# Kernel optimization log

Hardware: AMD Instinct MI355X
Metric: run time of the kernel (lower is better)

The kernel has to match this reference:

```python
import jax, jax.numpy as jnp
import numpy as np

N = 8192       # num_nodes
DEG = 16       # edges per node
E = N * DEG    # num_edges
F = 128        # num_features
R = 20         # num_rbf_features
L = 3          # num_message_passing_layers
CUT = 3.0      # cutoff_dist


def setup_inputs() -> dict:
    key = jax.random.key(0)
    ks = jax.random.split(key, 18)
    atoms = jax.random.randint(ks[0], (N,), 1, 119)
    # every node appears as a destination exactly DEG times -> bincount > 0
    idx_i = jnp.repeat(jnp.arange(N), DEG)
    idx_j = jax.random.randint(ks[1], (E,), 0, N)
    raw = jax.random.normal(ks[2], (E, 3), jnp.float32)
    rel_dir = raw / jnp.linalg.norm(raw, axis=-1, keepdims=True)
    rel_dist = jax.random.uniform(ks[3], (E,), jnp.float32, 0.1, CUT - 1e-3)
    emb = (jax.random.normal(ks[4], (119, F), jnp.float32) / np.sqrt(F)).at[0].set(0.0)
    def w(k, shape, fan_in):
        return jax.random.normal(k, shape, jnp.float32) / np.sqrt(fan_in)
    return {
        'atoms': atoms, 'idx_i': idx_i, 'idx_j': idx_j,
        'rel_dir': rel_dir, 'rel_dist': rel_dist, 'emb': emb,
        'msg_w1': w(ks[5], (L, F, F), F), 'msg_b1': jnp.zeros((L, F), jnp.float32),
        'msg_w2': w(ks[6], (L, F, 3 * F), F), 'msg_b2': jnp.zeros((L, 3 * F), jnp.float32),
        'rbf_w': w(ks[7], (L, R, 3 * F), R), 'rbf_b': jnp.zeros((L, 3 * F), jnp.float32),
        'Uw': w(ks[8], (L, F, F), F), 'Vw': w(ks[9], (L, F, F), F),
        'upd_w1': w(ks[10], (L, 2 * F, F), 2 * F), 'upd_b1': jnp.zeros((L, F), jnp.float32),
        'upd_w2': w(ks[11], (L, F, 3 * F), F), 'upd_b2': jnp.zeros((L, 3 * F), jnp.float32),
    }


def painn_forward(atoms, idx_i, idx_j, rel_dir, rel_dist, emb,
                  msg_w1, msg_b1, msg_w2, msg_b2, rbf_w, rbf_b,
                  Uw, Vw, upd_w1, upd_b1, upd_w2, upd_b2):
    silu = jax.nn.silu
    # cosine cutoff and sinusoidal RBF features of edge distances
    cut = 0.5 * (jnp.cos(jnp.pi * rel_dist / CUT) + 1.0)               # [E]
    n = jnp.arange(1, R + 1, dtype=rel_dist.dtype)
    rbf = jnp.sin(n * jnp.pi * rel_dist[:, None] / CUT) / rel_dist[:, None]  # [E,R]

    s = emb[atoms]                                   # [N,F]
    v = jnp.zeros((N, F, 3), s.dtype)                # [N,F,3]
    counts = jax.ops.segment_sum(jnp.ones(E, s.dtype), idx_i, num_segments=N)  # bincount

    for l in range(L):
        # ---- message block ----
        phi = silu(s @ msg_w1[l] + msg_b1[l]) @ msg_w2[l] + msg_b2[l]  # [N,3F]
        W = (rbf @ rbf_w[l] + rbf_b[l]) * cut[:, None]                 # [E,3F]
        phi_W = phi[idx_j] * W                                         # [E,3F]
        p_vv, p_ss, p_vs = jnp.split(phi_W, 3, axis=-1)
        ds = jax.ops.segment_sum(p_ss, idx_i, num_segments=N) / counts[:, None]
        ve = v[idx_j] * p_vv[..., None] + p_vs[..., None] * rel_dir[:, None, :]  # [E,F,3]
        dv = jax.ops.segment_sum(ve, idx_i, num_segments=N) / counts[:, None, None]
        s = s + ds
        v = v + dv
        # ---- update block ----
        Uv = jnp.einsum('nfc,fg->ngc', v, Uw[l])       # [N,F,3]
        Vv = jnp.einsum('nfc,fg->ngc', v, Vw[l])       # [N,F,3]
        a_in = jnp.concatenate([jnp.linalg.norm(Vv, axis=-1), s], axis=-1)  # [N,2F]
        a = silu(a_in @ upd_w1[l] + upd_b1[l]) @ upd_w2[l] + upd_b2[l]      # [N,3F]
        a_vv, a_sv, a_ss = jnp.split(a, 3, axis=-1)
        s = s + a_ss + a_sv * jnp.sum(Uv * Vv, axis=-1)
        v = v + Uv * a_vv[..., None]
    return s, v


def reference(atoms, idx_i, idx_j, rel_dir, rel_dist, emb,
              msg_w1, msg_b1, msg_w2, msg_b2, rbf_w, rbf_b,
              Uw, Vw, upd_w1, upd_b1, upd_w2, upd_b2):
    return painn_forward(atoms, idx_i, idx_j, rel_dir, rel_dist, emb,
                         msg_w1, msg_b1, msg_w2, msg_b2, rbf_w, rbf_b,
                         Uw, Vw, upd_w1, upd_b1, upd_w2, upd_b2)
```

## Files before the change

kernel.cpp:

```cpp
#include <hip/hip_runtime.h>
#include <hip/hip_fp16.h>

#define N_NODES 8192
#define DEG     16
#define NEDGE   (N_NODES*DEG)
#define F       128
#define F3      384
#define RBF     20
#define NLAYER  3
#define NF      (N_NODES*F)
#define PI_F    3.14159265358979f

typedef unsigned short u16;
typedef __bf16 bf16x8 __attribute__((ext_vector_type(8)));
typedef float  f32x4  __attribute__((ext_vector_type(4)));
typedef _Float16 f16x2 __attribute__((ext_vector_type(2)));

__device__ __forceinline__ float bf2f(u16 u){ return __uint_as_float(((unsigned)u)<<16); }
__device__ __forceinline__ u16 f2bf(float f){
  unsigned x = __float_as_uint(f);
  unsigned r = (x + 0x7FFFu + ((x>>16)&1u)) >> 16;
  return (u16)r;
}
__device__ __forceinline__ float lo_bf(unsigned u){ return __uint_as_float(u<<16); }
__device__ __forceinline__ float hi_bf(unsigned u){ return __uint_as_float(u & 0xFFFF0000u); }
__device__ __forceinline__ float silu_f(float x){ return x / (1.f + __expf(-x)); }
__device__ __forceinline__ float ldsrc(const void* src, int i, int bf){
  return bf ? bf2f(((const u16*)src)[i]) : ((const float*)src)[i];
}
__device__ __forceinline__ unsigned packh2(float a, float b){
  return (unsigned)__half_as_ushort(__float2half(a)) |
         ((unsigned)__half_as_ushort(__float2half(b)) << 16);
}
__device__ __forceinline__ float fdot2u(unsigned a, unsigned b, float c){
  return __builtin_amdgcn_fdot2(__builtin_bit_cast(f16x2, a),
                                __builtin_bit_cast(f16x2, b), c, false);
}

__global__ void k_detect(const u16* __restrict__ rd, int* __restrict__ flag){
  if (threadIdx.x == 0 && blockIdx.x == 0){
    int ok = 1;
    for (int i = 0; i < 128; i++){
      float v = bf2f(rd[2*i]);
      if (!(v > 0.01f && v < 4.0f)) { ok = 0; break; }
    }
    *flag = ok;
  }
}

__device__ __forceinline__ void splitw(const void* src, u16* bh, u16* bl,
                                       int i, int K, int Ncol, int bf){
  int kn = K*Ncol; int l = i/kn; int r = i - l*kn; int k = r/Ncol; int n = r - k*Ncol;
  float w = ldsrc(src, i, bf);
  u16 h = f2bf(w);
  size_t o = (size_t)l*kn + (size_t)n*K + k;
  bh[o] = h; bl[o] = f2bf(w - bf2f(h));
}

__global__ __launch_bounds__(256) void k_prep(
    const void* mb1, const void* mb2, const void* b1, const void* b2,
    const void* rw,  const void* rb,
    const void* mw1, const void* mw2, const void* w1, const void* w2,
    const void* Uw,  const void* Vw,
    const void* dist, const void* dirv, const int* __restrict__ idxj,
    const int* __restrict__ atoms, const void* __restrict__ emb,
    float* c_mb1, float* c_mb2, float* c_b1, float* c_b2,
    unsigned* rwp2,
    u16* mw1h, u16* mw1l, u16* mw2h, u16* mw2l, u16* w1h, u16* w1l,
    u16* w2h, u16* w2l, u16* uvh, u16* uvl,
    uint4* edata,
    float* s, u16* s_h, u16* s_l,
    u16* p0h, u16* p0l, u16* bufA16, u16* bufB16,
    const int* __restrict__ flag){
  int i = blockIdx.x*256 + threadIdx.x;
  int bf = *flag;
  const int S0=NLAYER*F, S1=NLAYER*F3, S2=NLAYER*F, S3=NLAYER*F3;
  const int S4=NLAYER*11*F3;
  const int S5=NLAYER*F*F, S6=NLAYER*F*F3, S7=NLAYER*2*F*F, S8=NLAYER*F*F3, S9=NLAYER*256*F;
  if (i < S0){ c_mb1[i]=ldsrc(mb1,i,bf); return; } i-=S0;
  if (i < S1){ c_mb2[i]=ldsrc(mb2,i,bf); return; } i-=S1;
  if (i < S2){ c_b1[i] =ldsrc(b1, i,bf); return; } i-=S2;
  if (i < S3){ c_b2[i] =ldsrc(b2, i,bf); return; } i-=S3;
  if (i < S4){
    int l = i/(11*F3); int r = i - l*(11*F3); int r2 = r/F3; int col = r - r2*F3;
    float w0, w1v;
    if (r2 < 10){
      w0  = ldsrc(rw, (l*RBF + 2*r2  )*F3 + col, bf);
      w1v = ldsrc(rw, (l*RBF + 2*r2+1)*F3 + col, bf);
    } else {
      w0  = ldsrc(rb, l*F3 + col, bf);
      w1v = 0.f;
    }
    rwp2[i] = packh2(w0, w1v);
    return;
  } i-=S4;
  if (i < S5){ splitw(mw1, mw1h, mw1l, i, F,   F,  bf); return; } i-=S5;
  if (i < S6){ splitw(mw2, mw2h, mw2l, i, F,   F3, bf); return; } i-=S6;
  if (i < S7){ splitw(w1,  w1h,  w1l,  i, 2*F, F,  bf); return; } i-=S7;
  if (i < S8){ splitw(w2,  w2h,  w2l,  i, F,   F3, bf); return; } i-=S8;
  if (i < S9){
    int l=i/(256*F); int r=i-l*(256*F); int n=r>>7; int k=r&127;
    int si=(l*F+k)*F+(n&127);
    float w = ldsrc((n<128)?Uw:Vw, si, bf);
    u16 h=f2bf(w); uvh[i]=h; uvl[i]=f2bf(w-bf2f(h));
    return;
  } i-=S9;
  if (i < NEDGE){
    int e = i;
    float d = ldsrc(dist, e, bf);
    float cut = 0.5f*(cosf(PI_F*d*(1.f/3.f)) + 1.0f);
    float ic = cut/d;
    unsigned o[16];
    #pragma unroll
    for (int r2=0;r2<10;r2++){
      float s0 = sinf((2*r2+1)*PI_F*d*(1.f/3.f))*ic;
      float s1 = sinf((2*r2+2)*PI_F*d*(1.f/3.f))*ic;
      o[r2] = packh2(s0, s1);
    }
    o[10] = packh2(cut, 0.f);
    o[11] = __float_as_uint(ldsrc(dirv, e*3+0, bf));
    o[12] = __float_as_uint(ldsrc(dirv, e*3+1, bf));
    o[13] = __float_as_uint(ldsrc(dirv, e*3+2, bf));
    o[14] = (unsigned)idxj[e];
    o[15] = 0;
    uint4* dst = edata + (size_t)e*4;
    dst[0] = make_uint4(o[0],o[1],o[2],o[3]);
    dst[1] = make_uint4(o[4],o[5],o[6],o[7]);
    dst[2] = make_uint4(o[8],o[9],o[10],o[11]);
    dst[3] = make_uint4(o[12],o[13],o[14],o[15]);
    return;
  } i-=NEDGE;
  if (i < NF){
    int n = i >> 7, f = i & 127;
    float sv = ldsrc(emb, atoms[n]*F + f, bf);
    s[i] = sv;
    u16 hb = f2bf(sv); s_h[i] = hb; s_l[i] = f2bf(sv - bf2f(hb));
    p0h[i]=0; p0h[NF+i]=0; p0h[2*(size_t)NF+i]=0;
    p0l[i]=0; p0l[NF+i]=0; p0l[2*(size_t)NF+i]=0;
    bufA16[(size_t)i*4+2]=0; bufA16[(size_t)i*4+3]=0;
    bufB16[(size_t)i*2+1]=0;
  }
}
#define PREP_TOTAL (NLAYER*(F+F3+F+F3+11*F3+F*F+F*F3+2*F*F+F*F3+256*F) + NEDGE + NF)

__global__ __launch_bounds__(256) void k_msg(const u16* __restrict__ s_h,
                                             const u16* __restrict__ s_l,
                                             const u16* __restrict__ w1h_,
                                             const u16* __restrict__ w1l_,
                                             const u16* __restrict__ w2h_,
                                             const u16* __restrict__ w2l_,
                                             const float* __restrict__ b1,
                                             const float* __restrict__ b2,
                                             u16* __restrict__ bufA16,
                                             u16* __restrict__ bufB16){
  __shared__ u16 Ah[16*136], Al[16*136];
  __shared__ u16 Hh[16*136], Hl[16*136];
  __shared__ u16 Bh[64*136], Bl[64*136];
  int t = threadIdx.x, lane = t&63, w = t>>6;
  int row0 = blockIdx.x<<4;
  int l15 = lane&15, q8 = (lane>>4)<<3, qrow = (lane>>4)<<2;

  #pragma unroll
  for (int q=0;q<2;q++){
    int id = t + 256*q; int pl = id>>8, rem = id&255, r = rem>>4, c = (rem&15)<<3;
    *(uint4*)((pl?Al:Ah)+r*136+c) = *(const uint4*)((pl?s_l:s_h) + (size_t)(row0+r)*F + c);
  }

  for (int cg=0;cg<2;cg++){
    __syncthreads();
    #pragma unroll
    for (int q=0;q<8;q++){
      int id = t + 256*q; int pl = id>>10, rem = id&1023, r = rem>>4, c = (rem&15)<<3;
      *(uint4*)((pl?Bl:Bh)+r*136+c) = *(const uint4*)((pl?w1l_:w1h_) + (size_t)(cg*64+r)*F + c);
    }
    __syncthreads();
    f32x4 acc; acc[0]=0;acc[1]=0;acc[2]=0;acc[3]=0;
    #pragma unroll
    for (int k0=0;k0<F;k0+=32){
      bf16x8 a_h = *(const bf16x8*)&Ah[l15*136 + k0 + q8];
      bf16x8 a_l = *(const bf16x8*)&Al[l15*136 + k0 + q8];
      bf16x8 b_h = *(const bf16x8*)&Bh[(w*16+l15)*136 + k0 + q8];
      bf16x8 b_l = *(const bf16x8*)&Bl[(w*16+l15)*136 + k0 + q8];
      acc = __builtin_amdgcn_mfma_f32_16x16x32_bf16(a_h, b_h, acc, 0,0,0);
      acc = __builtin_amdgcn_mfma_f32_16x16x32_bf16(a_h, b_l, acc, 0,0,0);
      acc = __builtin_amdgcn_mfma_f32_16x16x32_bf16(a_l, b_h, acc, 0,0,0);
    }
    int col = cg*64 + w*16 + l15;
    float bb = b1[col];
    #pragma unroll
    for (int r=0;r<4;r++){
      float val = silu_f(acc[r] + bb);
      u16 hb = f2bf(val);
      Hh[(qrow+r)*136 + col] = hb;
      Hl[(qrow+r)*136 + col] = f2bf(val - bf2f(hb));
    }
  }

  for (int cg=0;cg<6;cg++){
    __syncthreads();
    #pragma unroll
    for (int q=0;q<8;q++){
      int id = t + 256*q; int pl = id>>10, rem = id&1023, r = rem>>4, c = (rem&15)<<3;
      *(uint4*)((pl?Bl:Bh)+r*136+c) = *(const uint4*)((pl?w2l_:w2h_) + (size_t)(cg*64+r)*F + c);
    }
    __syncthreads();
    f32x4 acc; acc[0]=0;acc[1]=0;acc[2]=0;acc[3]=0;
    #pragma unroll
    for (int k0=0;k0<F;k0+=32){
      bf16x8 a_h = *(const bf16x8*)&Hh[l15*136 + k0 + q8];
      bf16x8 a_l = *(const bf16x8*)&Hl[l15*136 + k0 + q8];
      bf16x8 b_h = *(const bf16x8*)&Bh[(w*16+l15)*136 + k0 + q8];
      bf16x8 b_l = *(const bf16x8*)&Bl[(w*16+l15)*136 + k0 + q8];
      acc = __builtin_amdgcn_mfma_f32_16x16x32_bf16(a_h, b_h, acc, 0,0,0);
      acc = __builtin_amdgcn_mfma_f32_16x16x32_bf16(a_h, b_l, acc, 0,0,0);
      acc = __builtin_amdgcn_mfma_f32_16x16x32_bf16(a_l, b_h, acc, 0,0,0);
    }
    int gc = cg*64 + w*16 + l15;
    float bb = b2[gc];
    #pragma unroll
    for (int r=0;r<4;r++){
      int grow = row0 + qrow + r;
      u16 v = f2bf(acc[r] + bb);
      size_t rowo = (size_t)grow*F;
      if (gc < F)        bufA16[(rowo + gc)*4 + 0]     = v;
      else if (gc < 2*F) bufA16[(rowo + gc - F)*4 + 1] = v;
      else               bufB16[(rowo + gc - 2*F)*2]   = v;
    }
  }
}

__global__ __launch_bounds__(256) void k_agg(const uint4* __restrict__ ed_g,
                                             const uint2* __restrict__ bufA,
                                             const unsigned* __restrict__ bufB,
                                             const unsigned* __restrict__ rwp2,
                                             const u16* __restrict__ vi_h,
                                             const u16* __restrict__ vi_l,
                                             u16* __restrict__ vo_h,
                                             u16* __restrict__ vo_l,
                                             float* __restrict__ s,
                                             u16* __restrict__ s_h,
                                             u16* __restrict__ s_l){
  __shared__ uint4 ed4[128];
  int t = threadIdx.x;
  int half = t >> 7, f = t & 127;

  unsigned rw2[3][11];
  #pragma unroll
  for (int r2=0;r2<11;r2++){
    rw2[0][r2] = rwp2[r2*F3 + f];
    rw2[1][r2] = rwp2[r2*F3 + F + f];
    rw2[2][r2] = rwp2[r2*F3 + 2*F + f];
  }

  int nA = blockIdx.x * 2;
  if (t < 128) ed4[t] = ed_g[(size_t)nA*64 + t];
  __syncthreads();

  int n = nA + half;
  int base = half*64;
  float ds=0.f, dv0=0.f, dv1=0.f, dv2=0.f;

  int j0 = (int)(ed4[base+3].z & (N_NODES-1));
  uint2    pa = bufA[(size_t)j0*F + f];
  unsigned pb = bufB[(size_t)j0*F + f];
  for (int el=0;el<DEG;el++){
    uint2 cpa = pa; unsigned cpb = pb;
    if (el+1 < DEG){
      int j1 = (int)(ed4[base+(el+1)*4+3].z & (N_NODES-1));
      pa = bufA[(size_t)j1*F + f];
      pb = bufB[(size_t)j1*F + f];
    }
    uint4 q0 = ed4[base+el*4+0];
    uint4 q1 = ed4[base+el*4+1];
    uint4 q2 = ed4[base+el*4+2];
    uint4 q3 = ed4[base+el*4+3];
    unsigned rc[11] = {q0.x,q0.y,q0.z,q0.w, q1.x,q1.y,q1.z,q1.w, q2.x,q2.y,q2.z};
    float Wvv = 0.f, Wss = 0.f, Wvs = 0.f;
    #pragma unroll
    for (int r2=0;r2<11;r2++){
      Wvv = fdot2u(rc[r2], rw2[0][r2], Wvv);
      Wss = fdot2u(rc[r2], rw2[1][r2], Wss);
      Wvs = fdot2u(rc[r2], rw2[2][r2], Wvs);
    }
    float pvv = Wvv*lo_bf(cpa.x), pss = Wss*hi_bf(cpa.x), pvs = Wvs*lo_bf(cpb);
    ds += pss;
    dv0 += lo_bf(cpa.y)*pvv + pvs*__uint_as_float(q2.w);
    dv1 += hi_bf(cpa.y)*pvv + pvs*__uint_as_float(q3.x);
    dv2 += hi_bf(cpb)  *pvv + pvs*__uint_as_float(q3.y);
  }
  size_t i = (size_t)n*F + f;
  const float inv = 1.f/DEG;
  float sv = s[i] + ds*inv;
  s[i] = sv;
  { u16 hb = f2bf(sv); s_h[i] = hb; s_l[i] = f2bf(sv - bf2f(hb)); }
  float o0 = bf2f(vi_h[i])              + bf2f(vi_l[i])              + dv0*inv;
  float o1 = bf2f(vi_h[NF+i])           + bf2f(vi_l[NF+i])           + dv1*inv;
  float o2 = bf2f(vi_h[2*(size_t)NF+i]) + bf2f(vi_l[2*(size_t)NF+i]) + dv2*inv;
  u16 h0=f2bf(o0), h1=f2bf(o1), h2=f2bf(o2);
  vo_h[i]=h0; vo_h[NF+i]=h1; vo_h[2*(size_t)NF+i]=h2;
  vo_l[i]=f2bf(o0-bf2f(h0)); vo_l[NF+i]=f2bf(o1-bf2f(h1)); vo_l[2*(size_t)NF+i]=f2bf(o2-bf2f(h2));
}

__global__ __launch_bounds__(256) void k_uvdot(const u16* __restrict__ voh,
                                               const u16* __restrict__ vol,
                                               const u16* __restrict__ Bh_g,
                                               const u16* __restrict__ Bl_g,
                                               const float* __restrict__ s,
                                               float* __restrict__ uvF,
                                               float* __restrict__ dot,
                                               u16* __restrict__ ai_h,
                                               u16* __restrict__ ai_l){
  __shared__ u16 Ah[32*40], Al[32*40], BUh[64*40], BUl[64*40], BVh[64*40], BVl[64*40];
  int t = threadIdx.x;
  int row0 = blockIdx.y<<5, c0 = blockIdx.x<<6;
  int lane = t&63, w = t>>6;
  int qr = (w>>1)<<4, qc = (w&1)<<5;
  int l15 = lane&15, q8 = (lane>>4)<<3;
  int qrow = (lane>>4)<<2;
  int ap = t>>7, arem = t&127, ar = arem>>2, ac = (arem&3)<<3;
  f32x4 dA[2], nA2[2];
  dA[0][0]=0;dA[0][1]=0;dA[0][2]=0;dA[0][3]=0; dA[1]=dA[0];
  nA2[0]=dA[0]; nA2[1]=dA[0];

  for (int c=0;c<3;c++){
    f32x4 aU[2], aV[2];
    aU[0][0]=0;aU[0][1]=0;aU[0][2]=0;aU[0][3]=0; aU[1]=aU[0];
    aV[0]=aU[0]; aV[1]=aU[0];
    const u16* Asrc = (ap ? vol : voh) + (size_t)c*NF + (size_t)(row0+ar)*F + ac;
    u16* Adst = (ap ? Al : Ah) + ar*40 + ac;
    for (int k0=0;k0<F;k0+=32){
      *(uint4*)Adst = *(const uint4*)(Asrc + k0);
      #pragma unroll
      for (int q=0;q<4;q++){
        int idx = t + 256*q;
        int bp = idx>>8, rem = idx&255, br = rem>>2, bc = (rem&3)<<3;
        int grow = ((bp>>1) ? 128 : 0) + c0 + br;
        const u16* Bsrc = ((bp&1) ? Bl_g : Bh_g) + (size_t)grow*F + k0 + bc;
        u16* Bdst;
        if (bp==0) Bdst = BUh; else if (bp==1) Bdst = BUl; else if (bp==2) Bdst = BVh; else Bdst = BVl;
        *(uint4*)(Bdst + br*40 + bc) = *(const uint4*)Bsrc;
      }
      __syncthreads();
      bf16x8 a_h = *(const bf16x8*)&Ah[(qr+l15)*40 + q8];
      bf16x8 a_l = *(const bf16x8*)&Al[(qr+l15)*40 + q8];
      #pragma unroll
      for (int nt=0;nt<2;nt++){
        int off = (qc+nt*16+l15)*40 + q8;
        bf16x8 bu_h = *(const bf16x8*)&BUh[off];
        bf16x8 bu_l = *(const bf16x8*)&BUl[off];
        bf16x8 bv_h = *(const bf16x8*)&BVh[off];
        bf16x8 bv_l = *(const bf16x8*)&BVl[off];
        aU[nt] = __builtin_amdgcn_mfma_f32_16x16x32_bf16(a_h, bu_h, aU[nt], 0,0,0);
        aU[nt] = __builtin_amdgcn_mfma_f32_16x16x32_bf16(a_h, bu_l, aU[nt], 0,0,0);
        aU[nt] = __builtin_amdgcn_mfma_f32_16x16x32_bf16(a_l, bu_h, aU[nt], 0,0,0);
        aV[nt] = __builtin_amdgcn_mfma_f32_16x16x32_bf16(a_h, bv_h, aV[nt], 0,0,0);
        aV[nt] = __builtin_amdgcn_mfma_f32_16x16x32_bf16(a_h, bv_l, aV[nt], 0,0,0);
        aV[nt] = __builtin_amdgcn_mfma_f32_16x16x32_bf16(a_l, bv_h, aV[nt], 0,0,0);
      }
      __syncthreads();
    }
    #pragma unroll
    for (int nt=0;nt<2;nt++){
      int gcol = c0 + qc + nt*16 + l15;
      #pragma unroll
      for (int r=0;r<4;r++){
        int grow = row0 + qr + qrow + r;
        float u = aU[nt][r], v = aV[nt][r];
        dA[nt][r] += u*v;
        nA2[nt][r] += v*v;
        uvF[(size_t)c*NF + (size_t)grow*F + gcol] = u;
      }
    }
  }
  #pragma unroll
  for (int nt=0;nt<2;nt++){
    int gcol = c0 + qc + nt*16 + l15;
    #pragma unroll
    for (int r=0;r<4;r++){
      int grow = row0 + qr + qrow + r;
      dot[(size_t)grow*F + gcol] = dA[nt][r];
      float vn = sqrtf(nA2[nt][r]);
      float sv = s[(size_t)grow*F + gcol];
      size_t b = (size_t)grow*256 + gcol;
      u16 h0 = f2bf(vn), h1 = f2bf(sv);
      ai_h[b] = h0;     ai_l[b] = f2bf(vn - bf2f(h0));
      ai_h[b+128] = h1; ai_l[b+128] = f2bf(sv - bf2f(h1));
    }
  }
}

__global__ __launch_bounds__(256) void k_upd(const u16* __restrict__ ai_h,
                                             const u16* __restrict__ ai_l,
                                             const u16* __restrict__ w1h_,
                                             const u16* __restrict__ w1l_,
                                             const u16* __restrict__ w2h_,
                                             const u16* __restrict__ w2l_,
                                             const float* __restrict__ b1,
                                             const float* __restrict__ b2,
                                             const float* __restrict__ dot,
                                             const float* __restrict__ uvF,
                                             float* __restrict__ s,
                                             u16* __restrict__ s_h,
                                             u16* __restrict__ s_l,
                                             u16* __restrict__ v_h,
                                             u16* __restrict__ v_l,
                                             u16* __restrict__ bufA16,
                                             u16* __restrict__ bufB16,
                                             float* __restrict__ out){
  __shared__ u16 Ah[16*264], Al[16*264];
  __shared__ u16 Hh[16*136], Hl[16*136];
  __shared__ u16 Bh[64*136], Bl[64*136];
  __shared__ __half aLDS[16*392];
  int t = threadIdx.x, lane = t&63, w = t>>6;
  int row0 = blockIdx.x<<4;
  int l15 = lane&15, q8 = (lane>>4)<<3, qrow = (lane>>4)<<2;

  #pragma unroll
  for (int q=0;q<4;q++){
    int id = t + 256*q; int pl = id>>9, rem = id&511, r = rem>>5, c = (rem&31)<<3;
    *(uint4*)((pl?Al:Ah)+r*264+c) = *(const uint4*)((pl?ai_l:ai_h) + (size_t)(row0+r)*256 + c);
  }

  for (int cg=0;cg<2;cg++){
    f32x4 acc; acc[0]=0;acc[1]=0;acc[2]=0;acc[3]=0;
    for (int kc=0;kc<4;kc++){
      __syncthreads();
      #pragma unroll
      for (int q=0;q<4;q++){
        int id = t + 256*q; int pl = id>>9, rem = id&511, r = rem>>3, c = (rem&7)<<3;
        *(uint4*)((pl?Bl:Bh)+r*136+c) =
            *(const uint4*)((pl?w1l_:w1h_) + (size_t)(cg*64+r)*256 + kc*64 + c);
      }
      __syncthreads();
      #pragma unroll
      for (int ks=0;ks<64;ks+=32){
        bf16x8 a_h = *(const bf16x8*)&Ah[l15*264 + kc*64 + ks + q8];
        bf16x8 a_l = *(const bf16x8*)&Al[l15*264 + kc*64 + ks + q8];
        bf16x8 b_h = *(const bf16x8*)&Bh[(w*16+l15)*136 + ks + q8];
        bf16x8 b_l = *(const bf16x8*)&Bl[(w*16+l15)*136 + ks + q8];
        acc = __builtin_amdgcn_mfma_f32_16x16x32_bf16(a_h, b_h, acc, 0,0,0);
        acc = __builtin_amdgcn_mfma_f32_16x16x32_bf16(a_h, b_l, acc, 0,0,0);
        acc = __builtin_amdgcn_mfma_f32_16x16x32_bf16(a_l, b_h, acc, 0,0,0);
      }
    }
    int col = cg*64 + w*16 + l15;
    float bb = b1[col];
    #pragma unroll
    for (int r=0;r<4;r++){
      float val = silu_f(acc[r] + bb);
      u16 hb = f2bf(val);
      Hh[(qrow+r)*136 + col] = hb;
      Hl[(qrow+r)*136 + col] = f2bf(val - bf2f(hb));
    }
  }

  for (int cg=0;cg<6;cg++){
    __syncthreads();
    #pragma unroll
    for (int q=0;q<8;q++){
      int id = t + 256*q; int pl = id>>10, rem = id&1023, r = rem>>4, c = (rem&15)<<3;
      *(uint4*)((pl?Bl:Bh)+r*136+c) = *(const uint4*)((pl?w2l_:w2h_) + (size_t)(cg*64+r)*F + c);
    }
    __syncthreads();
    f32x4 acc; acc[0]=0;acc[1]=0;acc[2]=0;acc[3]=0;
    #pragma unroll
    for (int k0=0;k0<F;k0+=32){
      bf16x8 a_h = *(const bf16x8*)&Hh[l15*136 + k0 + q8];
      bf16x8 a_l = *(const bf16x8*)&Hl[l15*136 + k0 + q8];
      bf16x8 b_h = *(const bf16x8*)&Bh[(w*16+l15)*136 + k0 + q8];
      bf16x8 b_l = *(const bf16x8*)&Bl[(w*16+l15)*136 + k0 + q8];
      acc = __builtin_amdgcn_mfma_f32_16x16x32_bf16(a_h, b_h, acc, 0,0,0);
      acc = __builtin_amdgcn_mfma_f32_16x16x32_bf16(a_h, b_l, acc, 0,0,0);
      acc = __builtin_amdgcn_mfma_f32_16x16x32_bf16(a_l, b_h, acc, 0,0,0);
    }
    int gc = cg*64 + w*16 + l15;
    float bb = b2[gc];
    #pragma unroll
    for (int r=0;r<4;r++)
      aLDS[(qrow+r)*392 + gc] = __float2half(acc[r] + bb);
  }
  __syncthreads();

  int f = t & 127, rh = (t>>7)*8;
  #pragma unroll
  for (int e=0;e<8;e++){
    int r = rh + e;
    int grow = row0 + r;
    size_t i = (size_t)grow*F + f;
    float avv = __half2float(aLDS[r*392 + f]);
    float asv = __half2float(aLDS[r*392 + F + f]);
    float ass = __half2float(aLDS[r*392 + 2*F + f]);
    float sv = s[i] + ass + asv*dot[i];
    s[i] = sv;
    u16 hb = f2bf(sv); s_h[i] = hb; s_l[i] = f2bf(sv - bf2f(hb));
    float nv0 = bf2f(v_h[i])              + bf2f(v_l[i])              + uvF[i]*avv;
    float nv1 = bf2f(v_h[NF+i])           + bf2f(v_l[NF+i])           + uvF[NF+i]*avv;
    float nv2 = bf2f(v_h[2*(size_t)NF+i]) + bf2f(v_l[2*(size_t)NF+i]) + uvF[2*(size_t)NF+i]*avv;
    u16 h0=f2bf(nv0), h1=f2bf(nv1), h2=f2bf(nv2);
    v_h[i]=h0; v_h[NF+i]=h1; v_h[2*(size_t)NF+i]=h2;
    v_l[i]=f2bf(nv0-bf2f(h0)); v_l[NF+i]=f2bf(nv1-bf2f(h1)); v_l[2*(size_t)NF+i]=f2bf(nv2-bf2f(h2));
    bufA16[(size_t)i*4+2] = h0; bufA16[(size_t)i*4+3] = h1;
    bufB16[(size_t)i*2+1] = h2;
    if (out){
      out[i] = sv;
      out[NF + (size_t)i*3 + 0] = nv0;
      out[NF + (size_t)i*3 + 1] = nv1;
      out[NF + (size_t)i*3 + 2] = nv2;
    }
  }
}

extern "C" void kernel_launch(void* const* d_in, const int* in_sizes, int n_in,
                              void* d_out, int out_size, void* d_ws, size_t ws_size,
                              hipStream_t stream) {
  const int* atoms   = (const int*)d_in[0];
  const int* idxj    = (const int*)d_in[2];

  float* W = (float*)d_ws;
  size_t off = 64;
  int* flag = (int*)d_ws;
  #define ALLOCF(name, cnt) float* name = W+off; off += (((cnt)+63)&~(size_t)63)
  #define ALLOCU(name, cnt) u16* name = (u16*)(W+off); off += ((((cnt)+1)/2+63)&~(size_t)63)
  ALLOCF(c_mb1, NLAYER*F);
  ALLOCF(c_mb2, NLAYER*F3);
  ALLOCF(c_b1,  NLAYER*F);
  ALLOCF(c_b2,  NLAYER*F3);
  unsigned* c_rwp2 = (unsigned*)(W+off); off += ((NLAYER*11*F3+63)&~(size_t)63);
  uint4* edata = (uint4*)(W+off); off += (size_t)NEDGE*16;
  ALLOCU(w_mw1h, NLAYER*F*F);   ALLOCU(w_mw1l, NLAYER*F*F);
  ALLOCU(w_mw2h, NLAYER*F*F3);  ALLOCU(w_mw2l, NLAYER*F*F3);
  ALLOCU(w_uvh,  NLAYER*256*F); ALLOCU(w_uvl,  NLAYER*256*F);
  ALLOCU(w_w1h,  NLAYER*F*256); ALLOCU(w_w1l,  NLAYER*F*256);
  ALLOCU(w_w2h,  NLAYER*F*F3);  ALLOCU(w_w2l,  NLAYER*F*F3);
  uint2* bufA = (uint2*)(W+off); off += (size_t)2*NF;
  unsigned* bufB = (unsigned*)(W+off); off += (size_t)NF;
  ALLOCU(p0h, (size_t)3*NF); ALLOCU(p0l, (size_t)3*NF);
  ALLOCU(p1h, (size_t)3*NF); ALLOCU(p1l, (size_t)3*NF);
  ALLOCU(s_h,  NF); ALLOCU(s_l,  NF);
  ALLOCU(ai_h, (size_t)2*NF); ALLOCU(ai_l, (size_t)2*NF);
  ALLOCF(s,    NF);
  ALLOCF(uvF,  (size_t)3*NF);
  ALLOCF(dotb, NF);

  k_detect<<<1, 64, 0, stream>>>((const u16*)d_in[4], flag);
  k_prep<<<(PREP_TOTAL+255)/256, 256, 0, stream>>>(
      d_in[7], d_in[9], d_in[15], d_in[17],
      d_in[10], d_in[11],
      d_in[6], d_in[8], d_in[14], d_in[16],
      d_in[12], d_in[13],
      d_in[4], d_in[3], idxj,
      atoms, d_in[5],
      c_mb1, c_mb2, c_b1, c_b2, c_rwp2,
      w_mw1h, w_mw1l, w_mw2h, w_mw2l, w_w1h, w_w1l,
      w_w2h, w_w2l, w_uvh, w_uvl, edata,
      s, s_h, s_l, p0h, p0l, (u16*)bufA, (u16*)bufB, flag);

  for (int l=0; l<NLAYER; l++){
    u16* vih = (l & 1) ? p1h : p0h;
    u16* vil = (l & 1) ? p1l : p0l;
    u16* voh = (l & 1) ? p0h : p1h;
    u16* vol = (l & 1) ? p0l : p1l;
    k_msg<<<N_NODES/16, 256, 0, stream>>>(
        s_h, s_l,
        w_mw1h + (size_t)l*F*F,  w_mw1l + (size_t)l*F*F,
        w_mw2h + (size_t)l*F*F3, w_mw2l + (size_t)l*F*F3,
        c_mb1 + (size_t)l*F, c_mb2 + (size_t)l*F3,
        (u16*)bufA, (u16*)bufB);
    k_agg<<<N_NODES/2, 256, 0, stream>>>(
        edata, bufA, bufB, c_rwp2 + (size_t)l*11*F3,
        vih, vil, voh, vol, s, s_h, s_l);
    k_uvdot<<<dim3(2, N_NODES/32), 256, 0, stream>>>(
        voh, vol, w_uvh + (size_t)l*256*F, w_uvl + (size_t)l*256*F,
        s, uvF, dotb, ai_h, ai_l);
    k_upd<<<N_NODES/16, 256, 0, stream>>>(
        ai_h, ai_l,
        w_w1h + (size_t)l*F*256, w_w1l + (size_t)l*F*256,
        w_w2h + (size_t)l*F*F3,  w_w2l + (size_t)l*F*F3,
        c_b1 + (size_t)l*F, c_b2 + (size_t)l*F3,
        dotb, uvF, s, s_h, s_l, voh, vol,
        (u16*)bufA, (u16*)bufB,
        (l == NLAYER-1) ? (float*)d_out : nullptr);
  }
}
```

Baseline: 385.2 us.

## Batch neighbour gathers in aggregation, store Uv in bf16, use sine recurrence for RBF

The aggregation kernel now issues all 16 neighbour gathers up front rather than prefetching one edge ahead, and it reads the RBF weights from global memory inside the loop instead of keeping them in registers. The Uv intermediate passed between k_uvdot and k_upd is stored as bf16 instead of fp32, which cuts that traffic by half but adds rounding error. The prep kernel now builds the sinusoidal RBF features with a Chebyshev sine recurrence and fast intrinsics instead of 20 sinf calls, which may reduce accuracy slightly.

```diff
diff --git a/kernel.cpp b/kernel.cpp
--- a/kernel.cpp
+++ b/kernel.cpp
@@ -108,15 +108,19 @@
   if (i < NEDGE){
     int e = i;
     float d = ldsrc(dist, e, bf);
-    float cut = 0.5f*(cosf(PI_F*d*(1.f/3.f)) + 1.0f);
+    float th = PI_F*d*(1.f/3.f);
+    float c  = __cosf(th);
+    float s1 = __sinf(th);
+    float cut = 0.5f*(c + 1.0f);
     float ic = cut/d;
+    float sk[RBF+1];
+    sk[0] = s1; float sm1 = 0.f, s0 = s1;
+    #pragma unroll
+    for (int k=1;k<=RBF;k++){ float sn = 2.f*c*s0 - sm1; sk[k-1] = s0; sm1 = s0; s0 = sn; }
     unsigned o[16];
     #pragma unroll
-    for (int r2=0;r2<10;r2++){
-      float s0 = sinf((2*r2+1)*PI_F*d*(1.f/3.f))*ic;
-      float s1 = sinf((2*r2+2)*PI_F*d*(1.f/3.f))*ic;
-      o[r2] = packh2(s0, s1);
-    }
+    for (int r2=0;r2<10;r2++)
+      o[r2] = packh2(sk[2*r2]*ic, sk[2*r2+1]*ic);
     o[10] = packh2(cut, 0.f);
     o[11] = __float_as_uint(ldsrc(dirv, e*3+0, bf));
     o[12] = __float_as_uint(ldsrc(dirv, e*3+1, bf));
@@ -244,32 +248,24 @@
   int t = threadIdx.x;
   int half = t >> 7, f = t & 127;
 
-  unsigned rw2[3][11];
-  #pragma unroll
-  for (int r2=0;r2<11;r2++){
-    rw2[0][r2] = rwp2[r2*F3 + f];
-    rw2[1][r2] = rwp2[r2*F3 + F + f];
-    rw2[2][r2] = rwp2[r2*F3 + 2*F + f];
-  }
-
   int nA = blockIdx.x * 2;
   if (t < 128) ed4[t] = ed_g[(size_t)nA*64 + t];
   __syncthreads();
 
   int n = nA + half;
   int base = half*64;
+
+  uint2 pa[DEG]; unsigned pb[DEG];
+  #pragma unroll
+  for (int el=0;el<DEG;el++){
+    int j = (int)(ed4[base+el*4+3].z & (N_NODES-1));
+    pa[el] = bufA[(size_t)j*F + f];
+    pb[el] = bufB[(size_t)j*F + f];
+  }
+
   float ds=0.f, dv0=0.f, dv1=0.f, dv2=0.f;
-
-  int j0 = (int)(ed4[base+3].z & (N_NODES-1));
-  uint2    pa = bufA[(size_t)j0*F + f];
-  unsigned pb = bufB[(size_t)j0*F + f];
+  #pragma unroll
   for (int el=0;el<DEG;el++){
-    uint2 cpa = pa; unsigned cpb = pb;
-    if (el+1 < DEG){
-      int j1 = (int)(ed4[base+(el+1)*4+3].z & (N_NODES-1));
-      pa = bufA[(size_t)j1*F + f];
-      pb = bufB[(size_t)j1*F + f];
-    }
     uint4 q0 = ed4[base+el*4+0];
     uint4 q1 = ed4[base+el*4+1];
     uint4 q2 = ed4[base+el*4+2];
@@ -278,15 +274,15 @@
     float Wvv = 0.f, Wss = 0.f, Wvs = 0.f;
     #pragma unroll
     for (int r2=0;r2<11;r2++){
-      Wvv = fdot2u(rc[r2], rw2[0][r2], Wvv);
-      Wss = fdot2u(rc[r2], rw2[1][r2], Wss);
-      Wvs = fdot2u(rc[r2], rw2[2][r2], Wvs);
-    }
-    float pvv = Wvv*lo_bf(cpa.x), pss = Wss*hi_bf(cpa.x), pvs = Wvs*lo_bf(cpb);
+      Wvv = fdot2u(rc[r2], rwp2[r2*F3 + f],       Wvv);
+      Wss = fdot2u(rc[r2], rwp2[r2*F3 + F + f],   Wss);
+      Wvs = fdot2u(rc[r2], rwp2[r2*F3 + 2*F + f], Wvs);
+    }
+    float pvv = Wvv*lo_bf(pa[el].x), pss = Wss*hi_bf(pa[el].x), pvs = Wvs*lo_bf(pb[el]);
     ds += pss;
-    dv0 += lo_bf(cpa.y)*pvv + pvs*__uint_as_float(q2.w);
-    dv1 += hi_bf(cpa.y)*pvv + pvs*__uint_as_float(q3.x);
-    dv2 += hi_bf(cpb)  *pvv + pvs*__uint_as_float(q3.y);
+    dv0 += lo_bf(pa[el].y)*pvv + pvs*__uint_as_float(q2.w);
+    dv1 += hi_bf(pa[el].y)*pvv + pvs*__uint_as_float(q3.x);
+    dv2 += hi_bf(pb[el])  *pvv + pvs*__uint_as_float(q3.y);
   }
   size_t i = (size_t)n*F + f;
   const float inv = 1.f/DEG;
@@ -306,7 +302,7 @@
                                                const u16* __restrict__ Bh_g,
                                                const u16* __restrict__ Bl_g,
                                                const float* __restrict__ s,
-                                               float* __restrict__ uvF,
+                                               u16* __restrict__ uvFb,
                                                float* __restrict__ dot,
                                                u16* __restrict__ ai_h,
                                                u16* __restrict__ ai_l){
@@ -368,7 +364,7 @@
         float u = aU[nt][r], v = aV[nt][r];
         dA[nt][r] += u*v;
         nA2[nt][r] += v*v;
-        uvF[(size_t)c*NF + (size_t)grow*F + gcol] = u;
+        uvFb[(size_t)c*NF + (size_t)grow*F + gcol] = f2bf(u);
       }
     }
   }
@@ -398,7 +394,7 @@
                                              const float* __restrict__ b1,
                                              const float* __restrict__ b2,
                                              const float* __restrict__ dot,
-                                             const float* __restrict__ uvF,
+                                             const u16* __restrict__ uvFb,
                                              float* __restrict__ s,
                                              u16* __restrict__ s_h,
                                              u16* __restrict__ s_l,
@@ -493,9 +489,9 @@
     float sv = s[i] + ass + asv*dot[i];
     s[i] = sv;
     u16 hb = f2bf(sv); s_h[i] = hb; s_l[i] = f2bf(sv - bf2f(hb));
-    float nv0 = bf2f(v_h[i])              + bf2f(v_l[i])              + uvF[i]*avv;
-    float nv1 = bf2f(v_h[NF+i])           + bf2f(v_l[NF+i])           + uvF[NF+i]*avv;
-    float nv2 = bf2f(v_h[2*(size_t)NF+i]) + bf2f(v_l[2*(size_t)NF+i]) + uvF[2*(size_t)NF+i]*avv;
+    float nv0 = bf2f(v_h[i])              + bf2f(v_l[i])              + bf2f(uvFb[i])*avv;
+    float nv1 = bf2f(v_h[NF+i])           + bf2f(v_l[NF+i])           + bf2f(uvFb[NF+i])*avv;
+    float nv2 = bf2f(v_h[2*(size_t)NF+i]) + bf2f(v_l[2*(size_t)NF+i]) + bf2f(uvFb[2*(size_t)NF+i])*avv;
     u16 h0=f2bf(nv0), h1=f2bf(nv1), h2=f2bf(nv2);
     v_h[i]=h0; v_h[NF+i]=h1; v_h[2*(size_t)NF+i]=h2;
     v_l[i]=f2bf(nv0-bf2f(h0)); v_l[NF+i]=f2bf(nv1-bf2f(h1)); v_l[2*(size_t)NF+i]=f2bf(nv2-bf2f(h2));
@@ -538,8 +534,8 @@
   ALLOCU(p1h, (size_t)3*NF); ALLOCU(p1l, (size_t)3*NF);
   ALLOCU(s_h,  NF); ALLOCU(s_l,  NF);
   ALLOCU(ai_h, (size_t)2*NF); ALLOCU(ai_l, (size_t)2*NF);
+  ALLOCU(uvFb, (size_t)3*NF);
   ALLOCF(s,    NF);
-  ALLOCF(uvF,  (size_t)3*NF);
   ALLOCF(dotb, NF);
 
   k_detect<<<1, 64, 0, stream>>>((const u16*)d_in[4], flag);
@@ -571,13 +567,13 @@
         vih, vil, voh, vol, s, s_h, s_l);
     k_uvdot<<<dim3(2, N_NODES/32), 256, 0, stream>>>(
         voh, vol, w_uvh + (size_t)l*256*F, w_uvl + (size_t)l*256*F,
-        s, uvF, dotb, ai_h, ai_l);
+        s, uvFb, dotb, ai_h, ai_l);
     k_upd<<<N_NODES/16, 256, 0, stream>>>(
         ai_h, ai_l,
         w_w1h + (size_t)l*F*256, w_w1l + (size_t)l*F*256,
         w_w2h + (size_t)l*F*F3,  w_w2l + (size_t)l*F*F3,
         c_b1 + (size_t)l*F, c_b2 + (size_t)l*F3,
-        dotb, uvF, s, s_h, s_l, voh, vol,
+        dotb, uvFb, s, s_h, s_l, voh, vol,
         (u16*)bufA, (u16*)bufB,
         (l == NLAYER-1) ? (float*)d_out : nullptr);
   }
```

After: 427.6 us. +11.0%, slower.
